# Kernel optimization log

Measured on AMD Instinct MI355X. Metric: run time of the kernel, lower is better.

The kernel has to match this reference:

```python
import jax, jax.numpy as jnp
import numpy as np
jax.config.update("jax_enable_x64", True)

B, N, S, H, D = 64, 13, 128, 768, 512
MAX_DEPTH = 8
MAX_SHAPE_IDS = 256  # min(2**13, 256)


def _gelu(x):
    return jax.nn.gelu(x, approximate=False)  # torch nn.GELU default (erf)


def setup_inputs() -> dict:
    key = jax.random.key(0)
    ks = jax.random.split(key, 12)
    # BFS-complete binary tree with 13 nodes: nodes 0..5 internal, 6..12 leaves
    left = np.array([2 * i + 1 if 2 * i + 2 < N else -1 for i in range(N)], dtype=np.int64)
    right = np.array([2 * i + 2 if 2 * i + 2 < N else -1 for i in range(N)], dtype=np.int64)
    depth = np.array([int(np.floor(np.log2(i + 1))) for i in range(N)], dtype=np.int64)
    is_leaf = np.tile((left == -1)[None, :], (B, 1))  # (B, N) bool
    active = np.ones((B, N), dtype=bool)
    leaf_states = jax.random.normal(ks[0], (B, N, S, H), dtype=jnp.float32)
    leaf_masks = jax.random.bernoulli(ks[1], 0.8, (B, N, S))  # bool
    s = 0.02
    params = dict(
        Wl1=jax.random.normal(ks[2], (H, D), dtype=jnp.float32) * s,
        bl1=jnp.zeros((D,), jnp.float32),
        Wl2=jax.random.normal(ks[3], (D, D), dtype=jnp.float32) * s,
        bl2=jnp.zeros((D,), jnp.float32),
        Wm1=jax.random.normal(ks[4], (2 * D, D), dtype=jnp.float32) * s,
        bm1=jnp.zeros((D,), jnp.float32),
        Wm2=jax.random.normal(ks[5], (D, D), dtype=jnp.float32) * s,
        bm2=jnp.zeros((D,), jnp.float32),
        depth_emb=jax.random.normal(ks[6], (MAX_DEPTH, D), dtype=jnp.float32) * s,
        shape_emb=jax.random.normal(ks[7], (MAX_SHAPE_IDS, D), dtype=jnp.float32) * s,
    )
    return dict(is_leaf=is_leaf, active=active, depth=depth, left_child=left,
                right_child=right, leaf_states=leaf_states, leaf_masks=leaf_masks,
                **params)


def reference(is_leaf, active, depth, left_child, right_child, leaf_states, leaf_masks,
              Wl1, bl1, Wl2, bl2, Wm1, bm1, Wm2, bm2, depth_emb, shape_emb):
    is_leaf = jnp.asarray(is_leaf)
    active = jnp.asarray(active)
    # --- leaf pass (vectorized over all nodes) ---
    maskf = leaf_masks[..., None].astype(leaf_states.dtype)          # (B,N,S,1)
    pooled = (leaf_states * maskf).sum(2) / jnp.maximum(maskf.sum(2), 1.0)  # (B,N,H)
    enc = _gelu(pooled @ Wl1 + bl1) @ Wl2 + bl2                       # (B,N,D)
    enc = enc + depth_emb[jnp.asarray(depth)][None, :, :]             # per-node depth embed
    node_repr = enc * is_leaf[..., None].astype(enc.dtype)            # zero non-leaves
    # --- bottom-up merge (small fixed loop over max_nodes, reverse BFS) ---
    lc_np = np.asarray(left_child)
    rc_np = np.asarray(right_child)
    dp_np = np.asarray(depth)
    for i in range(N - 1, -1, -1):
        lc, rc = int(lc_np[i]), int(rc_np[i])
        if lc == -1:
            continue
        is_internal = active[:, i] & ~is_leaf[:, i]                   # (B,)
        cat = jnp.concatenate([node_repr[:, lc], node_repr[:, rc]], axis=-1)  # (B,2D)
        merged = _gelu(cat @ Wm1 + bm1) @ Wm2 + bm2 + depth_emb[int(dp_np[i])]
        # torch code overwrites the whole column with merged*mask iff any internal
        col = jnp.where(jnp.any(is_internal),
                        merged * is_internal[:, None].astype(merged.dtype),
                        node_repr[:, i])
        node_repr = node_repr.at[:, i].set(col)
    # --- topology hash -> shape embedding ---
    pattern = active.astype(jnp.int64) * 2 + is_leaf.astype(jnp.int64)  # (B,N)
    weights = jnp.array([31 ** i for i in range(N)], dtype=jnp.int64)    # fits int64 for N<=13
    hashed = jnp.abs((pattern * weights[None, :]).sum(1)) % MAX_SHAPE_IDS
    return node_repr[:, 0] + shape_emb[hashed]
```

## Files before the change

### kernel.cpp

```cpp
#include <hip/hip_runtime.h>
#include <hip/hip_bf16.h>
#include <math.h>

#define NN 13
#define SS 128
#define HH 768
#define DD 512

typedef __attribute__((ext_vector_type(8))) short bf16x8;
typedef __attribute__((ext_vector_type(4))) float f32x4;

__device__ __forceinline__ float gelu_f(float x) {
    return 0.5f * x * (1.0f + erff(x * 0.7071067811865475f));
}
__device__ __forceinline__ ushort f2b(float v) {
    __hip_bfloat16 h = __float2bfloat16(v);
    return *reinterpret_cast<ushort*>(&h);
}
__device__ __forceinline__ float b2f(ushort u) {
    __hip_bfloat16 h = *reinterpret_cast<__hip_bfloat16*>(&u);
    return __bfloat162float(h);
}

__device__ __forceinline__ int shape_hash(const int* __restrict__ active,
                                          const int* __restrict__ is_leaf, int b) {
    unsigned long long acc = 0ull, w = 1ull;
    for (int i = 0; i < NN; ++i) {
        unsigned long long p = (unsigned long long)(active[b*NN + i] * 2 + is_leaf[b*NN + i]);
        acc += p * w;
        w *= 31ull;
    }
    long long h = (long long)acc;
    if (h < 0) h = -h;
    return (int)(h % 256);
}

__global__ __launch_bounds__(256)
void pool_transpose(const float* __restrict__ ls, const int* __restrict__ masks,
                    const int* __restrict__ is_leaf, ushort* __restrict__ pooled,
                    const float* __restrict__ Wl1, const float* __restrict__ Wl2,
                    const float* __restrict__ Wm1, const float* __restrict__ Wm2,
                    ushort* __restrict__ Tl1, ushort* __restrict__ Tl2,
                    ushort* __restrict__ Tm1, ushort* __restrict__ Tm2)
{
    int bx = blockIdx.x;
    int t = threadIdx.x;
    if (bx < 2496) {
        if (t >= 64) return;
        int u = bx / 3, q = bx - u*3;
        int n = u >> 6, b = u & 63;
        int c = q*64 + t;
        ushort4* dst = (ushort4*)(pooled + (size_t)u * HH);
        if (!is_leaf[b*NN + n]) {
            ushort4 z = {0,0,0,0};
            dst[c] = z;
            return;
        }
        __shared__ float lsm[SS];
        const int* mk = masks + (b*NN + n)*SS;
        lsm[t] = (float)mk[t];
        lsm[64 + t] = (float)mk[64 + t];
        __syncthreads();
        const float4* src = (const float4*)(ls + (size_t)(b*NN + n) * SS * HH);
        float4 a = {0.f, 0.f, 0.f, 0.f};
        float cnt = 0.f;
        #pragma unroll 8
        for (int s = 0; s < SS; ++s) {
            float m = lsm[s];
            float4 v = src[(size_t)s * (HH/4) + c];
            a.x += m * v.x; a.y += m * v.y; a.z += m * v.z; a.w += m * v.w;
            cnt += m;
        }
        float inv = 1.f / fmaxf(cnt, 1.f);
        ushort4 o = { f2b(a.x*inv), f2b(a.y*inv), f2b(a.z*inv), f2b(a.w*inv) };
        dst[c] = o;
        return;
    }
    int tb = bx - 2496;
    const float* W; ushort* T; int K, tile;
    if (tb < 384)       { W = Wl1; T = Tl1; K = 768;  tile = tb; }
    else if (tb < 640)  { W = Wl2; T = Tl2; K = 512;  tile = tb - 384; }
    else if (tb < 1152) { W = Wm1; T = Tm1; K = 1024; tile = tb - 640; }
    else                { W = Wm2; T = Tm2; K = 512;  tile = tb - 1152; }
    int tk = tile >> 4, tj = tile & 15;
    __shared__ float lds[32][33];
    int r = t >> 3, c0 = (t & 7) * 4;
    const float4 v = *(const float4*)(W + (size_t)(tk*32 + r)*DD + tj*32 + c0);
    lds[r][c0+0] = v.x; lds[r][c0+1] = v.y; lds[r][c0+2] = v.z; lds[r][c0+3] = v.w;
    __syncthreads();
    ushort* dst = T + (size_t)(tj*32 + r)*K + tk*32 + c0;
    dst[0] = f2b(lds[c0+0][r]); dst[1] = f2b(lds[c0+1][r]);
    dst[2] = f2b(lds[c0+2][r]); dst[3] = f2b(lds[c0+3][r]);
}

enum { LEAF_G1 = 0, LEAF_G2 = 1, MERGE_G1 = 2, MERGE_G2 = 3, FINAL_G2 = 4 };

template<int MODE, int KT>
__global__ __launch_bounds__(256)
void mfma_gemm(const ushort* __restrict__ Asrc, const ushort* __restrict__ WT,
               const float* __restrict__ bias, void* __restrict__ CoutV,
               const int* __restrict__ is_leaf, const int* __restrict__ active,
               const int* __restrict__ depth, const int* __restrict__ left,
               const int* __restrict__ right,
               const float* __restrict__ depth_emb, const float* __restrict__ shape_emb,
               const ushort* __restrict__ noderep,
               int n0, int n1, int n2)
{
    constexpr int NITER = KT / 32;
    __shared__ ushort a_lds[2][64*40];
    __shared__ ushort b_lds[2][64*40];

    const int t = threadIdx.x;
    const int lane = t & 63, wv = t >> 6;
    const int j0 = blockIdx.x * 64;
    const int by = blockIdx.y;
    const int lrow = lane & 15, lhi = lane >> 4;

    int node, lc = 0, rc = 0;
    if (MODE == LEAF_G1 || MODE == LEAF_G2) {
        node = by;
        bool anyleaf = __any(is_leaf[lane*NN + node] != 0);
        if (!anyleaf) {
            if (MODE == LEAF_G2) {
                ushort* dst = (ushort*)CoutV + (size_t)(node*64)*DD;
                #pragma unroll
                for (int c = 0; c < 4; ++c) {
                    int jc = j0 + c*16 + lrow;
                    #pragma unroll
                    for (int reg = 0; reg < 4; ++reg) {
                        int rw = wv*16 + lhi*4 + reg;
                        dst[(size_t)rw*DD + jc] = 0;
                    }
                }
            }
            return;
        }
    } else {
        node = (by == 0) ? n0 : ((by == 1) ? n1 : n2);
        lc = left[node]; rc = right[node];
    }

    const int AK = (MODE == LEAF_G1) ? HH : DD;
    const int rowbase = (MODE == LEAF_G1 || MODE == LEAF_G2) ? node*64
                       : (MODE == MERGE_G1) ? 0 : by*64;

    const int sr = t >> 2, skg = t & 3;
    f32x4 acc[4];
    #pragma unroll
    for (int c = 0; c < 4; ++c) acc[c] = (f32x4){0.f, 0.f, 0.f, 0.f};

    auto addrA = [&](int kt) -> const ushort* {
        int k0 = kt*32 + skg*8;
        if (MODE == MERGE_G1) {
            return (k0 < DD) ? noderep + (size_t)(lc*64 + sr)*DD + k0
                             : noderep + (size_t)(rc*64 + sr)*DD + (k0 - DD);
        }
        return Asrc + (size_t)(rowbase + sr)*AK + k0;
    };
    auto addrB = [&](int kt) -> const ushort* {
        return WT + (size_t)(j0 + sr)*KT + kt*32 + skg*8;
    };

    uint4 aR0, bR0, aR1, bR1;
    auto load0 = [&](int kt) { aR0 = *(const uint4*)addrA(kt); bR0 = *(const uint4*)addrB(kt); };
    auto load1 = [&](int kt) { aR1 = *(const uint4*)addrA(kt); bR1 = *(const uint4*)addrB(kt); };
    auto store0 = [&](int buf) {
        *(uint4*)&a_lds[buf][sr*40 + skg*8] = aR0;
        *(uint4*)&b_lds[buf][sr*40 + skg*8] = bR0;
    };
    auto store1 = [&](int buf) {
        *(uint4*)&a_lds[buf][sr*40 + skg*8] = aR1;
        *(uint4*)&b_lds[buf][sr*40 + skg*8] = bR1;
    };
    auto computeOn = [&](const ushort* aL, const ushort* bL) {
        bf16x8 af = *(const bf16x8*)&aL[(wv*16 + lrow)*40 + lhi*8];
        #pragma unroll
        for (int c = 0; c < 4; ++c) {
            bf16x8 bfr = *(const bf16x8*)&bL[(c*16 + lrow)*40 + lhi*8];
            acc[c] = __builtin_amdgcn_mfma_f32_16x16x32_bf16(af, bfr, acc[c], 0, 0, 0);
        }
    };

    load0(0);
    store0(0);
    if (NITER > 1) load1(1);
    __syncthreads();

    for (int kt = 0; kt < NITER; kt += 2) {
        computeOn(a_lds[0], b_lds[0]);
        if (kt + 2 < NITER) load0(kt + 2);
        store1(1);
        __syncthreads();
        computeOn(a_lds[1], b_lds[1]);
        if (kt + 3 < NITER) load1(kt + 3);
        if (kt + 2 < NITER) store0(0);
        __syncthreads();
    }

    if (MODE == LEAF_G1) {
        ushort* H = (ushort*)CoutV + (size_t)(node*64)*DD;
        #pragma unroll
        for (int c = 0; c < 4; ++c) {
            int jc = j0 + c*16 + lrow;
            float bj = bias[jc];
            #pragma unroll
            for (int reg = 0; reg < 4; ++reg) {
                int rw = wv*16 + lhi*4 + reg;
                H[(size_t)rw*DD + jc] = f2b(gelu_f(acc[c][reg] + bj));
            }
        }
    } else if (MODE == LEAF_G2) {
        int dp = depth[node];
        const float* de = depth_emb + (size_t)dp*DD;
        bool lf[4];
        #pragma unroll
        for (int reg = 0; reg < 4; ++reg)
            lf[reg] = is_leaf[(wv*16 + lhi*4 + reg)*NN + node] != 0;
        ushort* dst = (ushort*)CoutV + (size_t)(node*64)*DD;
        #pragma unroll
        for (int c = 0; c < 4; ++c) {
            int jc = j0 + c*16 + lrow;
            float bj = bias[jc] + de[jc];
            #pragma unroll
            for (int reg = 0; reg < 4; ++reg) {
                int rw = wv*16 + lhi*4 + reg;
                dst[(size_t)rw*DD + jc] = f2b(lf[reg] ? (acc[c][reg] + bj) : 0.f);
            }
        }
    } else if (MODE == MERGE_G1) {
        ushort* Mh = (ushort*)CoutV + (size_t)(by*64)*DD;
        #pragma unroll
        for (int c = 0; c < 4; ++c) {
            int jc = j0 + c*16 + lrow;
            float bj = bias[jc];
            #pragma unroll
            for (int reg = 0; reg < 4; ++reg) {
                int rw = wv*16 + lhi*4 + reg;
                Mh[(size_t)rw*DD + jc] = f2b(gelu_f(acc[c][reg] + bj));
            }
        }
    } else {
        int dp = depth[node];
        const float* de = depth_emb + (size_t)dp*DD;
        bool anyInt = __any(active[lane*NN + node] && !is_leaf[lane*NN + node]);
        bool iv[4];
        #pragma unroll
        for (int reg = 0; reg < 4; ++reg) {
            int rw = wv*16 + lhi*4 + reg;
            iv[reg] = active[rw*NN + node] && !is_leaf[rw*NN + node];
        }
        if (MODE == MERGE_G2) {
            if (!anyInt) return;
            ushort* dst = (ushort*)CoutV + (size_t)(node*64)*DD;
            #pragma unroll
            for (int c = 0; c < 4; ++c) {
                int jc = j0 + c*16 + lrow;
                float bj = bias[jc] + de[jc];
                #pragma unroll
                for (int reg = 0; reg < 4; ++reg) {
                    int rw = wv*16 + lhi*4 + reg;
                    dst[(size_t)rw*DD + jc] = f2b(iv[reg] ? (acc[c][reg] + bj) : 0.f);
                }
            }
        } else {
            float* out = (float*)CoutV;
            int hh[4];
            #pragma unroll
            for (int reg = 0; reg < 4; ++reg)
                hh[reg] = shape_hash(active, is_leaf, wv*16 + lhi*4 + reg);
            #pragma unroll
            for (int c = 0; c < 4; ++c) {
                int jc = j0 + c*16 + lrow;
                float bj = bias[jc] + de[jc];
                #pragma unroll
                for (int reg = 0; reg < 4; ++reg) {
                    int rw = wv*16 + lhi*4 + reg;
                    float base = anyInt ? (iv[reg] ? (acc[c][reg] + bj) : 0.f)
                                        : b2f(noderep[(size_t)(node*64 + rw)*DD + jc]);
                    out[(size_t)rw*DD + jc] = base + shape_emb[(size_t)hh[reg]*DD + jc];
                }
            }
        }
    }
}

extern "C" void kernel_launch(void* const* d_in, const int* in_sizes, int n_in,
                              void* d_out, int out_size, void* d_ws, size_t ws_size,
                              hipStream_t stream)
{
    const int*   is_leaf     = (const int*)d_in[0];
    const int*   active      = (const int*)d_in[1];
    const int*   depth       = (const int*)d_in[2];
    const int*   left        = (const int*)d_in[3];
    const int*   right       = (const int*)d_in[4];
    const float* leaf_states = (const float*)d_in[5];
    const int*   leaf_masks  = (const int*)d_in[6];
    const float* Wl1 = (const float*)d_in[7];
    const float* bl1 = (const float*)d_in[8];
    const float* Wl2 = (const float*)d_in[9];
    const float* bl2 = (const float*)d_in[10];
    const float* Wm1 = (const float*)d_in[11];
    const float* bm1 = (const float*)d_in[12];
    const float* Wm2 = (const float*)d_in[13];
    const float* bm2 = (const float*)d_in[14];
    const float* depth_emb = (const float*)d_in[15];
    const float* shape_emb = (const float*)d_in[16];
    float* out = (float*)d_out;

    ushort* pooled  = (ushort*)d_ws;
    ushort* hidden  = pooled + 832*768;
    ushort* noderep = hidden + 832*512;
    ushort* mhid    = noderep + 832*512;
    ushort* Tl1 = mhid + 3*64*512;
    ushort* Tl2 = Tl1 + 512*768;
    ushort* Tm1 = Tl2 + 512*512;
    ushort* Tm2 = Tm1 + 512*1024;

    pool_transpose<<<2496 + 1408, 256, 0, stream>>>(leaf_states, leaf_masks, is_leaf, pooled,
                                                    Wl1, Wl2, Wm1, Wm2, Tl1, Tl2, Tm1, Tm2);

    mfma_gemm<LEAF_G1, 768><<<dim3(8, 13), 256, 0, stream>>>(
        pooled, Tl1, bl1, hidden, is_leaf, active, depth, left, right,
        depth_emb, shape_emb, noderep, 0, 0, 0);
    mfma_gemm<LEAF_G2, 512><<<dim3(8, 13), 256, 0, stream>>>(
        hidden, Tl2, bl2, noderep, is_leaf, active, depth, left, right,
        depth_emb, shape_emb, noderep, 0, 0, 0);

    mfma_gemm<MERGE_G1, 1024><<<dim3(8, 3), 256, 0, stream>>>(
        nullptr, Tm1, bm1, mhid, is_leaf, active, depth, left, right,
        depth_emb, shape_emb, noderep, 3, 4, 5);
    mfma_gemm<MERGE_G2, 512><<<dim3(8, 3), 256, 0, stream>>>(
        mhid, Tm2, bm2, noderep, is_leaf, active, depth, left, right,
        depth_emb, shape_emb, noderep, 3, 4, 5);

    mfma_gemm<MERGE_G1, 1024><<<dim3(8, 2), 256, 0, stream>>>(
        nullptr, Tm1, bm1, mhid, is_leaf, active, depth, left, right,
        depth_emb, shape_emb, noderep, 1, 2, 0);
    mfma_gemm<MERGE_G2, 512><<<dim3(8, 2), 256, 0, stream>>>(
        mhid, Tm2, bm2, noderep, is_leaf, active, depth, left, right,
        depth_emb, shape_emb, noderep, 1, 2, 0);

    mfma_gemm<MERGE_G1, 1024><<<dim3(8, 1), 256, 0, stream>>>(
        nullptr, Tm1, bm1, mhid, is_leaf, active, depth, left, right,
        depth_emb, shape_emb, noderep, 0, 0, 0);
    mfma_gemm<FINAL_G2, 512><<<dim3(8, 1), 256, 0, stream>>>(
        mhid, Tm2, bm2, out, is_leaf, active, depth, left, right,
        depth_emb, shape_emb, noderep, 0, 0, 0);
}
```

Measured before the change: 99.04 us.

## Fuse the eight GEMM launches into one cooperative kernel with grid syncs

The separate leaf and merge GEMM launches become a single cooperative kernel of 104 blocks. Each stage runs on a subset of blocks, and grid.sync() separates the stages so there is no per-launch gap and no kernel-boundary drain. In exchange, idle blocks spin at every barrier and each stage's parallelism is still limited to the blocks it uses. The kernel also relies on cooperative launch being supported.

```diff
diff --git a/kernel.cpp b/kernel.cpp
--- a/kernel.cpp
+++ b/kernel.cpp
@@ -1,4 +1,5 @@
 #include <hip/hip_runtime.h>
+#include <hip/hip_cooperative_groups.h>
 #include <hip/hip_bf16.h>
 #include <math.h>
 
@@ -96,24 +97,22 @@
 enum { LEAF_G1 = 0, LEAF_G2 = 1, MERGE_G1 = 2, MERGE_G2 = 3, FINAL_G2 = 4 };
 
 template<int MODE, int KT>
-__global__ __launch_bounds__(256)
-void mfma_gemm(const ushort* __restrict__ Asrc, const ushort* __restrict__ WT,
-               const float* __restrict__ bias, void* __restrict__ CoutV,
-               const int* __restrict__ is_leaf, const int* __restrict__ active,
-               const int* __restrict__ depth, const int* __restrict__ left,
-               const int* __restrict__ right,
-               const float* __restrict__ depth_emb, const float* __restrict__ shape_emb,
-               const ushort* __restrict__ noderep,
-               int n0, int n1, int n2)
+__device__ __forceinline__ void gemm_body(
+    int bx, ushort (&a_lds)[2][64*40], ushort (&b_lds)[2][64*40],
+    const ushort* __restrict__ Asrc, const ushort* __restrict__ WT,
+    const float* __restrict__ bias, void* __restrict__ CoutV,
+    const int* __restrict__ is_leaf, const int* __restrict__ active,
+    const int* __restrict__ depth, const int* __restrict__ left,
+    const int* __restrict__ right,
+    const float* __restrict__ depth_emb, const float* __restrict__ shape_emb,
+    const ushort* __restrict__ noderep,
+    int n0, int n1, int n2)
 {
     constexpr int NITER = KT / 32;
-    __shared__ ushort a_lds[2][64*40];
-    __shared__ ushort b_lds[2][64*40];
-
     const int t = threadIdx.x;
     const int lane = t & 63, wv = t >> 6;
-    const int j0 = blockIdx.x * 64;
-    const int by = blockIdx.y;
+    const int j0 = (bx & 7) * 64;
+    const int by = bx >> 3;
     const int lrow = lane & 15, lhi = lane >> 4;
 
     int node, lc = 0, rc = 0;
@@ -282,6 +281,53 @@
             }
         }
     }
+}
+
+__global__ __launch_bounds__(256)
+void mega_gemm(const ushort* pooled, const ushort* Tl1, const float* bl1, ushort* hidden,
+               const ushort* Tl2, const float* bl2, ushort* noderep,
+               const ushort* Tm1, const float* bm1, ushort* mhid,
+               const ushort* Tm2, const float* bm2, float* out,
+               const int* is_leaf, const int* active, const int* depth,
+               const int* left, const int* right,
+               const float* depth_emb, const float* shape_emb)
+{
+    __shared__ ushort a_lds[2][64*40];
+    __shared__ ushort b_lds[2][64*40];
+    cooperative_groups::grid_group grid = cooperative_groups::this_grid();
+    const int bx = blockIdx.x;
+
+    if (bx < 104) gemm_body<LEAF_G1, 768>(bx, a_lds, b_lds, pooled, Tl1, bl1, hidden,
+                                          is_leaf, active, depth, left, right,
+                                          depth_emb, shape_emb, noderep, 0, 0, 0);
+    grid.sync();
+    if (bx < 104) gemm_body<LEAF_G2, 512>(bx, a_lds, b_lds, hidden, Tl2, bl2, noderep,
+                                          is_leaf, active, depth, left, right,
+                                          depth_emb, shape_emb, noderep, 0, 0, 0);
+    grid.sync();
+    if (bx < 24)  gemm_body<MERGE_G1, 1024>(bx, a_lds, b_lds, nullptr, Tm1, bm1, mhid,
+                                            is_leaf, active, depth, left, right,
+                                            depth_emb, shape_emb, noderep, 3, 4, 5);
+    grid.sync();
+    if (bx < 24)  gemm_body<MERGE_G2, 512>(bx, a_lds, b_lds, mhid, Tm2, bm2, noderep,
+                                           is_leaf, active, depth, left, right,
+                                           depth_emb, shape_emb, noderep, 3, 4, 5);
+    grid.sync();
+    if (bx < 16)  gemm_body<MERGE_G1, 1024>(bx, a_lds, b_lds, nullptr, Tm1, bm1, mhid,
+                                            is_leaf, active, depth, left, right,
+                                            depth_emb, shape_emb, noderep, 1, 2, 0);
+    grid.sync();
+    if (bx < 16)  gemm_body<MERGE_G2, 512>(bx, a_lds, b_lds, mhid, Tm2, bm2, noderep,
+                                           is_leaf, active, depth, left, right,
+                                           depth_emb, shape_emb, noderep, 1, 2, 0);
+    grid.sync();
+    if (bx < 8)   gemm_body<MERGE_G1, 1024>(bx, a_lds, b_lds, nullptr, Tm1, bm1, mhid,
+                                            is_leaf, active, depth, left, right,
+                                            depth_emb, shape_emb, noderep, 0, 0, 0);
+    grid.sync();
+    if (bx < 8)   gemm_body<FINAL_G2, 512>(bx, a_lds, b_lds, mhid, Tm2, bm2, out,
+                                           is_leaf, active, depth, left, right,
+                                           depth_emb, shape_emb, noderep, 0, 0, 0);
 }
 
 extern "C" void kernel_launch(void* const* d_in, const int* in_sizes, int n_in,
@@ -319,31 +365,18 @@
     pool_transpose<<<2496 + 1408, 256, 0, stream>>>(leaf_states, leaf_masks, is_leaf, pooled,
                                                     Wl1, Wl2, Wm1, Wm2, Tl1, Tl2, Tm1, Tm2);
 
-    mfma_gemm<LEAF_G1, 768><<<dim3(8, 13), 256, 0, stream>>>(
-        pooled, Tl1, bl1, hidden, is_leaf, active, depth, left, right,
-        depth_emb, shape_emb, noderep, 0, 0, 0);
-    mfma_gemm<LEAF_G2, 512><<<dim3(8, 13), 256, 0, stream>>>(
-        hidden, Tl2, bl2, noderep, is_leaf, active, depth, left, right,
-        depth_emb, shape_emb, noderep, 0, 0, 0);
-
-    mfma_gemm<MERGE_G1, 1024><<<dim3(8, 3), 256, 0, stream>>>(
-        nullptr, Tm1, bm1, mhid, is_leaf, active, depth, left, right,
-        depth_emb, shape_emb, noderep, 3, 4, 5);
-    mfma_gemm<MERGE_G2, 512><<<dim3(8, 3), 256, 0, stream>>>(
-        mhid, Tm2, bm2, noderep, is_leaf, active, depth, left, right,
-        depth_emb, shape_emb, noderep, 3, 4, 5);
-
-    mfma_gemm<MERGE_G1, 1024><<<dim3(8, 2), 256, 0, stream>>>(
-        nullptr, Tm1, bm1, mhid, is_leaf, active, depth, left, right,
-        depth_emb, shape_emb, noderep, 1, 2, 0);
-    mfma_gemm<MERGE_G2, 512><<<dim3(8, 2), 256, 0, stream>>>(
-        mhid, Tm2, bm2, noderep, is_leaf, active, depth, left, right,
-        depth_emb, shape_emb, noderep, 1, 2, 0);
-
-    mfma_gemm<MERGE_G1, 1024><<<dim3(8, 1), 256, 0, stream>>>(
-        nullptr, Tm1, bm1, mhid, is_leaf, active, depth, left, right,
-        depth_emb, shape_emb, noderep, 0, 0, 0);
-    mfma_gemm<FINAL_G2, 512><<<dim3(8, 1), 256, 0, stream>>>(
-        mhid, Tm2, bm2, out, is_leaf, active, depth, left, right,
-        depth_emb, shape_emb, noderep, 0, 0, 0);
-}
+    const ushort* c_pooled = pooled;
+    const ushort* c_Tl1 = Tl1; const ushort* c_Tl2 = Tl2;
+    const ushort* c_Tm1 = Tm1; const ushort* c_Tm2 = Tm2;
+    void* args[] = {
+        (void*)&c_pooled, (void*)&c_Tl1, (void*)&bl1, (void*)&hidden,
+        (void*)&c_Tl2, (void*)&bl2, (void*)&noderep,
+        (void*)&c_Tm1, (void*)&bm1, (void*)&mhid,
+        (void*)&c_Tm2, (void*)&bm2, (void*)&out,
+        (void*)&is_leaf, (void*)&active, (void*)&depth,
+        (void*)&left, (void*)&right,
+        (void*)&depth_emb, (void*)&shape_emb
+    };
+    hipLaunchCooperativeKernel((const void*)mega_gemm, dim3(104), dim3(256),
+                               args, 0, stream);
+}
```

Result: slower. 183.7 us (+85.5%).
